# Optimization experiments

Hardware: AMD Instinct MI355X
Metric: run time of the kernel (lower is better)

## Reference

```python
import jax, jax.numpy as jnp
import numpy as np

NCAMS1, NIDENT1 = 40, 256
NCAMS2, NIDENT2 = 80, 512


def setup_inputs() -> dict:
    key = jax.random.key(0)
    k_img, k_cam, k_id, k_dt = jax.random.split(key, 4)
    B, C, H, W = 16, 3, 1024, 1024
    image = jax.random.normal(k_img, (B, C, H, W), dtype=jnp.float32)
    camindex = jax.random.randint(k_cam, (B,), 0, NCAMS1, dtype=jnp.int32)
    idindex = jax.random.randint(k_id, (B,), 0, NIDENT1, dtype=jnp.int32)
    dataset_type = jax.random.randint(k_dt, (B,), 0, 2, dtype=jnp.int32)
    # parameters (match torch init: wcam=ones, others zeros); perturb slightly so math is non-trivial
    kp = jax.random.split(jax.random.key(1), 8)
    params = {
        'wcam1': jnp.ones((NCAMS1, 3), jnp.float32) + 0.01 * jax.random.normal(kp[0], (NCAMS1, 3)),
        'bcam1': 0.01 * jax.random.normal(kp[1], (NCAMS1, 3)),
        'wident1': 0.01 * jax.random.normal(kp[2], (NIDENT1, 3)),
        'bident1': 0.01 * jax.random.normal(kp[3], (NIDENT1, 3)),
        'wcam2': jnp.ones((NCAMS2, 3), jnp.float32) + 0.01 * jax.random.normal(kp[4], (NCAMS2, 3)),
        'bcam2': 0.01 * jax.random.normal(kp[5], (NCAMS2, 3)),
        'wident2': 0.01 * jax.random.normal(kp[6], (NIDENT2, 3)),
        'bident2': 0.01 * jax.random.normal(kp[7], (NIDENT2, 3)),
    }
    return dict(image=image, camindex=camindex, idindex=idindex,
                dataset_type=dataset_type, **params)


def reference(image, camindex, idindex, dataset_type,
              wcam1, bcam1, wident1, bident1,
              wcam2, bcam2, wident2, bident2):
    # Vectorized version of the per-sample Python loop: for each sample select
    # dataset-1 or dataset-2 tables, gather per-(cam,id) affine params, apply.
    sel = (dataset_type == 0)[:, None]              # [B,1]
    w1 = wcam1[camindex] + wident1[idindex]         # [B,3]
    b1 = bcam1[camindex] + bident1[idindex]
    w2 = wcam2[camindex] + wident2[idindex]
    b2 = bcam2[camindex] + bident2[idindex]
    w = jnp.where(sel, w1, w2)                      # [B,3]
    b = jnp.where(sel, b1, b2)
    return w[:, :, None, None] * image + b[:, :, None, None]
```

## Files before the change

### kernel.cpp

```cpp
#include <hip/hip_runtime.h>


#define HW4 (1024 * 1024 / 4)

__global__ __launch_bounds__(256) void colorcal_kernel(
    const float* __restrict__ image,
    const int* __restrict__ camindex,
    const int* __restrict__ idindex,
    const int* __restrict__ dataset_type,
    const float* __restrict__ wcam1, const float* __restrict__ bcam1,
    const float* __restrict__ wident1, const float* __restrict__ bident1,
    const float* __restrict__ wcam2, const float* __restrict__ bcam2,
    const float* __restrict__ wident2, const float* __restrict__ bident2,
    float* __restrict__ out)
{
    const int plane = blockIdx.y;
    const int b = plane / 3;
    const int c = plane - b * 3;

    const int cam = camindex[b];
    const int id  = idindex[b];
    const int ds  = dataset_type[b];

    float w, bias;
    if (ds == 0) {
        w    = wcam1[cam * 3 + c] + wident1[id * 3 + c];
        bias = bcam1[cam * 3 + c] + bident1[id * 3 + c];
    } else {
        w    = wcam2[cam * 3 + c] + wident2[id * 3 + c];
        bias = bcam2[cam * 3 + c] + bident2[id * 3 + c];
    }

    const size_t base4 = (size_t)plane * HW4;
    const float4* __restrict__ in4  = reinterpret_cast<const float4*>(image) + base4;
    float4* __restrict__ out4 = reinterpret_cast<float4*>(out) + base4;

    const int i = blockIdx.x * blockDim.x + threadIdx.x;
    if (i < HW4) {
        float4 v = in4[i];
        float4 r;
        r.x = fmaf(w, v.x, bias);
        r.y = fmaf(w, v.y, bias);
        r.z = fmaf(w, v.z, bias);
        r.w = fmaf(w, v.w, bias);
        out4[i] = r;
    }
}

extern "C" void kernel_launch(void* const* d_in, const int* in_sizes, int n_in,
                              void* d_out, int out_size, void* d_ws, size_t ws_size,
                              hipStream_t stream) {
    const float* image        = (const float*)d_in[0];
    const int*   camindex     = (const int*)d_in[1];
    const int*   idindex      = (const int*)d_in[2];
    const int*   dataset_type = (const int*)d_in[3];
    const float* wcam1   = (const float*)d_in[4];
    const float* bcam1   = (const float*)d_in[5];
    const float* wident1 = (const float*)d_in[6];
    const float* bident1 = (const float*)d_in[7];
    const float* wcam2   = (const float*)d_in[8];
    const float* bcam2   = (const float*)d_in[9];
    const float* wident2 = (const float*)d_in[10];
    const float* bident2 = (const float*)d_in[11];
    float* out = (float*)d_out;

    const int planes = 16 * 3;
    dim3 grid((HW4 + 255) / 256, planes, 1);
    dim3 block(256, 1, 1);
    colorcal_kernel<<<grid, block, 0, stream>>>(
        image, camindex, idindex, dataset_type,
        wcam1, bcam1, wident1, bident1,
        wcam2, bcam2, wident2, bident2, out);
}
```

Baseline: 73.47 us.

## Process four vectors per thread with nontemporal loads and stores

Each thread now loads four float4 elements spaced one block apart, then computes and writes them using nontemporal builtins. The grid shrinks by four, so the per-block scalar parameter gather is amortized over more data, and the streaming hint is meant to avoid polluting caches. The bounds check is dropped because the plane size divides the tile size exactly.

```diff
diff --git a/kernel.cpp b/kernel.cpp
--- a/kernel.cpp
+++ b/kernel.cpp
@@ -1,9 +1,14 @@
 #include <hip/hip_runtime.h>
 
 
+typedef float fx4 __attribute__((ext_vector_type(4)));
+
 #define HW4 (1024 * 1024 / 4)
+#define VPT 4
+#define TPB 256
+#define TILE (TPB * VPT)
 
-__global__ __launch_bounds__(256) void colorcal_kernel(
+__global__ __launch_bounds__(TPB) void colorcal_kernel(
     const float* __restrict__ image,
     const int* __restrict__ camindex,
     const int* __restrict__ idindex,
@@ -31,19 +36,25 @@
         bias = bcam2[cam * 3 + c] + bident2[id * 3 + c];
     }
 
-    const size_t base4 = (size_t)plane * HW4;
-    const float4* __restrict__ in4  = reinterpret_cast<const float4*>(image) + base4;
-    float4* __restrict__ out4 = reinterpret_cast<float4*>(out) + base4;
+    const size_t base4 = (size_t)plane * HW4 + (size_t)blockIdx.x * TILE;
+    const fx4* __restrict__ in4  = reinterpret_cast<const fx4*>(image) + base4;
+    fx4* __restrict__ out4 = reinterpret_cast<fx4*>(out) + base4;
 
-    const int i = blockIdx.x * blockDim.x + threadIdx.x;
-    if (i < HW4) {
-        float4 v = in4[i];
-        float4 r;
-        r.x = fmaf(w, v.x, bias);
-        r.y = fmaf(w, v.y, bias);
-        r.z = fmaf(w, v.z, bias);
-        r.w = fmaf(w, v.w, bias);
-        out4[i] = r;
+    const int t = threadIdx.x;
+
+    fx4 v[VPT];
+#pragma unroll
+    for (int k = 0; k < VPT; ++k)
+        v[k] = __builtin_nontemporal_load(&in4[t + k * TPB]);
+
+#pragma unroll
+    for (int k = 0; k < VPT; ++k) {
+        fx4 r;
+        r.x = fmaf(w, v[k].x, bias);
+        r.y = fmaf(w, v[k].y, bias);
+        r.z = fmaf(w, v[k].z, bias);
+        r.w = fmaf(w, v[k].w, bias);
+        __builtin_nontemporal_store(r, &out4[t + k * TPB]);
     }
 }
 
@@ -65,8 +76,8 @@
     float* out = (float*)d_out;
 
     const int planes = 16 * 3;
-    dim3 grid((HW4 + 255) / 256, planes, 1);
-    dim3 block(256, 1, 1);
+    dim3 grid(HW4 / TILE, planes, 1);
+    dim3 block(TPB, 1, 1);
     colorcal_kernel<<<grid, block, 0, stream>>>(
         image, camindex, idindex, dataset_type,
         wcam1, bcam1, wident1, bident1,
```

Result: faster. 68.68 us (-6.5%).
